# Optimization experiments

Measured on AMD Instinct MI355X. Metric: run time of the kernel, lower is better.

The kernel has to match this reference:

```python
import jax, jax.numpy as jnp
import numpy as np

B, SQ, SK = 2, 2048, 2048
D = 1024            # in_features == num_heads * head_size
H, HS = 16, 64      # num_heads, head_size
SCALE = HS ** -0.5


def setup_inputs() -> dict:
    key = jax.random.key(0)
    ks = jax.random.split(key, 10)
    s = 0.02
    return {
        "inputs": jax.random.normal(ks[0], (B, SQ, D), jnp.float32),
        "context": jax.random.normal(ks[1], (B, SK, D), jnp.float32),
        "Wq": jax.random.normal(ks[2], (D, D), jnp.float32) * s,
        "bq": jnp.zeros((D,), jnp.float32),
        "Wk": jax.random.normal(ks[3], (D, D), jnp.float32) * s,
        "bk": jnp.zeros((D,), jnp.float32),
        "Wv": jax.random.normal(ks[4], (D, D), jnp.float32) * s,
        "bv": jnp.zeros((D,), jnp.float32),
        "Wo": jax.random.normal(ks[5], (D, D), jnp.float32) * s,
        "bo": jnp.zeros((D,), jnp.float32),
    }


def reference(inputs, context, Wq, bq, Wk, bk, Wv, bv, Wo, bo):
    # QKV projections (torch Linear: x @ W.T + b; here W stored as [in, out])
    q = inputs @ Wq + bq            # [B, SQ, D]
    k = context @ Wk + bk           # [B, SK, D]
    v = context @ Wv + bv           # [B, SK, D]
    q = q.reshape(B, SQ, H, HS)
    k = k.reshape(B, SK, H, HS)
    v = v.reshape(B, SK, H, HS)
    # scores: [B, H, SQ, SK] -- full score matrix materialized (as in source)
    score = jnp.einsum("bqhd,bkhd->bhqk", q, k) * SCALE
    weights = jax.nn.softmax(score, axis=-1)
    attn = jnp.einsum("bhqk,bkhd->bqhd", weights, v)  # [B, SQ, H, HS]
    out = attn.reshape(B, SQ, H * HS)
    return out @ Wo + bo
```

## Files before the change

kernel.cpp:

```cpp
#include <hip/hip_runtime.h>

#define BB 2
#define SQ 2048
#define SK 2048
#define DD 1024
#define HH 16
#define HS 64
#define SCALE 0.125f
#define LOG2E 1.4426950408889634f

typedef __bf16 bf16x8 __attribute__((ext_vector_type(8)));
typedef float f32x4 __attribute__((ext_vector_type(4)));
typedef unsigned int uint;

#if defined(__has_builtin)
#if __has_builtin(__builtin_amdgcn_exp2f)
#define FEXP2(x) __builtin_amdgcn_exp2f(x)
#endif
#endif
#ifndef FEXP2
extern "C" __device__ float __ocml_native_exp2_f32(float);
#define FEXP2(x) __ocml_native_exp2_f32(x)
#endif

__device__ __forceinline__ void gload_lds16(const __bf16* g, __bf16* l) {
    __builtin_amdgcn_global_load_lds((const __attribute__((address_space(1))) uint*)(g),
                                     (__attribute__((address_space(3))) uint*)(l), 16, 0, 0);
}

__global__ void wtrans(const float* __restrict__ W0, const float* __restrict__ W1,
                       const float* __restrict__ W2, const float* __restrict__ W3,
                       __bf16* __restrict__ Wt) {
    __shared__ __bf16 tile[32][33];
    const float* W = blockIdx.z == 0 ? W0 : blockIdx.z == 1 ? W1 : blockIdx.z == 2 ? W2 : W3;
    __bf16* out = Wt + (size_t)blockIdx.z * DD * DD;
    int tx = threadIdx.x, ty = threadIdx.y;
    int k0 = blockIdx.y * 32, n0 = blockIdx.x * 32;
#pragma unroll
    for (int j = 0; j < 4; ++j)
        tile[ty + j * 8][tx] = (__bf16)W[(size_t)(k0 + ty + j * 8) * DD + n0 + tx];
    __syncthreads();
#pragma unroll
    for (int j = 0; j < 4; ++j) {
        int n = n0 + ty + j * 8;
        int k = k0 + tx;
        int kswz = (k & ~63) | ((((k >> 3) ^ n) & 7) << 3) | (k & 7);
        out[(size_t)n * DD + kswz] = tile[tx][ty + j * 8];
    }
}

__global__ __launch_bounds__(256, 3) void gemm_qkv(
        const float* __restrict__ Ain, const float* __restrict__ Actx,
        const __bf16* __restrict__ Wt,
        const float* __restrict__ bq, const float* __restrict__ bk, const float* __restrict__ bv,
        __bf16* __restrict__ Qb, __bf16* __restrict__ Kb, __bf16* __restrict__ Vtb,
        float qscale) {
    __shared__ __bf16 As[128 * 64];
    __shared__ __bf16 Bs[128 * 64];
    int t = threadIdx.x, w = t >> 6, l = t & 63;
    int lm = l & 15, lk = l >> 4;
    int wr = w >> 1, wc = w & 1;
    int flat = blockIdx.x + 16 * blockIdx.y;
    int nf = (flat & 7) * 96 + (flat >> 3);
    bool isQ = nf < 256;
    int bc, br;
    if (isQ) { bc = nf & 7; br = nf >> 3; }
    else     { int f = nf - 256; bc = f & 15; br = f >> 4; }

    int rA = t >> 3, cA = t & 7;
    const float* Afp = isQ ? Ain : Actx;
    const float* agb = Afp + (size_t)(br * 128 + rA) * 1024 + cA * 8;
    __bf16* aw = &As[rA * 64 + ((cA ^ (rA & 7)) * 8)];

    const __bf16 *bg0, *bg1, *bg2, *bg3;
    if (isQ) {
        const __bf16* Wq_ = Wt;
        bg0 = Wq_ + (size_t)(bc * 128 + rA)      * 1024 + cA * 8;
        bg1 = Wq_ + (size_t)(bc * 128 + rA + 32) * 1024 + cA * 8;
        bg2 = Wq_ + (size_t)(bc * 128 + rA + 64) * 1024 + cA * 8;
        bg3 = Wq_ + (size_t)(bc * 128 + rA + 96) * 1024 + cA * 8;
    } else {
        const __bf16* Wk_ = Wt + (size_t)DD * DD;
        const __bf16* Wv_ = Wt + (size_t)2 * DD * DD;
        bg0 = Wk_ + (size_t)(bc * 64 + rA)      * 1024 + cA * 8;
        bg1 = Wk_ + (size_t)(bc * 64 + rA + 32) * 1024 + cA * 8;
        bg2 = Wv_ + (size_t)(bc * 64 + rA)      * 1024 + cA * 8;
        bg3 = Wv_ + (size_t)(bc * 64 + rA + 32) * 1024 + cA * 8;
    }
    __bf16* bw = &Bs[rA * 64 + cA * 8];

    int brow[4];
#pragma unroll
    for (int n = 0; n < 4; ++n)
        brow[n] = isQ ? (wc * 64 + n * 16 + lm)
                      : ((n >> 1) * 64 + wc * 32 + (n & 1) * 16 + lm);

    float4 a0l, a0h, a1l, a1h, a2l, a2h, a3l, a3h, xb0, xb1, xb2, xb3;
#define G_LOAD()                                                                      \
    a0l = *(const float4*)(agb);              a0h = *(const float4*)(agb + 4);        \
    a1l = *(const float4*)(agb + 32768);      a1h = *(const float4*)(agb + 32772);    \
    a2l = *(const float4*)(agb + 65536);      a2h = *(const float4*)(agb + 65540);    \
    a3l = *(const float4*)(agb + 98304);      a3h = *(const float4*)(agb + 98308);    \
    xb0 = *(const float4*)bg0; xb1 = *(const float4*)bg1;                             \
    xb2 = *(const float4*)bg2; xb3 = *(const float4*)bg3;                             \
    agb += 64; bg0 += 64; bg1 += 64; bg2 += 64; bg3 += 64;
#define CVT8(LO, HI) bf16x8{(__bf16)LO.x, (__bf16)LO.y, (__bf16)LO.z, (__bf16)LO.w,   \
                            (__bf16)HI.x, (__bf16)HI.y, (__bf16)HI.z, (__bf16)HI.w}
#define G_WRITE()                                                                     \
    {                                                                                 \
        *(bf16x8*)(aw)        = CVT8(a0l, a0h);                                       \
        *(bf16x8*)(aw + 2048) = CVT8(a1l, a1h);                                       \
        *(bf16x8*)(aw + 4096) = CVT8(a2l, a2h);                                       \
        *(bf16x8*)(aw + 6144) = CVT8(a3l, a3h);                                       \
        *(float4*)(bw)        = xb0;                                                  \
        *(float4*)(bw + 2048) = xb1;                                                  \
        *(float4*)(bw + 4096) = xb2;                                                  \
        *(float4*)(bw + 6144) = xb3;                                                  \
    }

    f32x4 acc[4][4] = {};
    G_LOAD();
    for (int ts = 0; ts < 16; ++ts) {
        __syncthreads();
        G_WRITE();
        __syncthreads();
        if (ts + 1 < 16) { G_LOAD(); }
#pragma unroll
        for (int kk = 0; kk < 2; ++kk) {
            int ch = kk * 4 + lk;
            bf16x8 af[4], bf[4];
#pragma unroll
            for (int m = 0; m < 4; ++m)
                af[m] = *(const bf16x8*)&As[(wr * 64 + m * 16 + lm) * 64 + ((ch ^ (lm & 7)) * 8)];
#pragma unroll
            for (int n = 0; n < 4; ++n)
                bf[n] = *(const bf16x8*)&Bs[brow[n] * 64 + ((ch ^ (lm & 7)) * 8)];
#pragma unroll
            for (int m = 0; m < 4; ++m)
#pragma unroll
                for (int n = 0; n < 4; ++n)
                    acc[m][n] = __builtin_amdgcn_mfma_f32_16x16x32_bf16(af[m], bf[n], acc[m][n], 0, 0, 0);
        }
    }
#undef G_LOAD
#undef G_WRITE
#undef CVT8

    if (isQ) {
#pragma unroll
        for (int m = 0; m < 4; ++m)
#pragma unroll
            for (int n = 0; n < 4; ++n) {
                int col = bc * 128 + wc * 64 + n * 16 + lm;
                float bb = bq[col];
#pragma unroll
                for (int r = 0; r < 4; ++r) {
                    int row = br * 128 + wr * 64 + m * 16 + lk * 4 + r;
                    Qb[(size_t)row * 1024 + col] = (__bf16)((acc[m][n][r] + bb) * qscale);
                }
            }
    } else {
#pragma unroll
        for (int m = 0; m < 4; ++m)
#pragma unroll
            for (int n = 0; n < 4; ++n) {
                int col = bc * 64 + wc * 32 + (n & 1) * 16 + lm;
                if (n < 2) {
                    float bb = bk[col];
#pragma unroll
                    for (int r = 0; r < 4; ++r) {
                        int row = br * 128 + wr * 64 + m * 16 + lk * 4 + r;
                        Kb[(size_t)row * 1024 + col] = (__bf16)(acc[m][n][r] + bb);
                    }
                } else {
                    float bb = bv[col];
                    int row = br * 128 + wr * 64 + m * 16 + lk * 4;
                    int b_ = row >> 11, sk = row & 2047;
                    int skb = sk & ~63, o = sk & 63;
                    int p0 = (o & 32) | (((o >> 3) & 1) << 4) | (((o >> 2) & 1) << 3) | (((o >> 4) & 1) << 2);
                    int h_ = col >> 6, d_ = col & 63;
                    union { ushort4 u; __bf16 hh[4]; } pk;
#pragma unroll
                    for (int r = 0; r < 4; ++r) pk.hh[r] = (__bf16)(acc[m][n][r] + bb);
                    *(ushort4*)(Vtb + ((size_t)((b_ * 16 + h_) * 64 + d_) * 2048 + skb + p0)) = pk.u;
                }
            }
    }
}

__global__ __launch_bounds__(256) void gemm_out64(const __bf16* __restrict__ A, const __bf16* __restrict__ Bt,
                                                  const float* __restrict__ bias, float* __restrict__ C) {
    __shared__ __bf16 As[64][64];
    __shared__ __bf16 Bs[128][64];
    int t = threadIdx.x;
    int w = t >> 6, l = t & 63;
    int lm = l & 15, lk = l >> 4;
    int flat = blockIdx.x + 8 * blockIdx.y;
    int nf = (flat & 7) * 64 + (flat >> 3);
    int bc = nf & 7, br = nf >> 3;
    int srow = (l >> 3), scol = (l & 7) * 8;
    f32x4 acc[4][2] = {};
    for (int kt = 0; kt < 1024; kt += 64) {
        __syncthreads();
#pragma unroll
        for (int j = 0; j < 2; ++j) {
            int r0 = (j * 4 + w) * 8;
            gload_lds16(&A[(size_t)(br * 64 + r0 + srow) * 1024 + kt + scol], &As[r0][0]);
        }
#pragma unroll
        for (int j = 0; j < 4; ++j) {
            int r0 = (j * 4 + w) * 8;
            gload_lds16(&Bt[(size_t)(bc * 128 + r0 + srow) * 1024 + kt + scol], &Bs[r0][0]);
        }
        __syncthreads();
#pragma unroll
        for (int kk = 0; kk < 64; kk += 32) {
            int ch = ((kk >> 3) + lk);
            bf16x8 af[4], bf[2];
#pragma unroll
            for (int m = 0; m < 4; ++m) af[m] = *(const bf16x8*)&As[m * 16 + lm][kk + lk * 8];
#pragma unroll
            for (int n = 0; n < 2; ++n)
                bf[n] = *(const bf16x8*)&Bs[w * 32 + n * 16 + lm][(ch ^ (lm & 7)) * 8];
#pragma unroll
            for (int m = 0; m < 4; ++m)
#pragma unroll
                for (int n = 0; n < 2; ++n)
                    acc[m][n] = __builtin_amdgcn_mfma_f32_16x16x32_bf16(af[m], bf[n], acc[m][n], 0, 0, 0);
        }
    }
#pragma unroll
    for (int m = 0; m < 4; ++m)
#pragma unroll
        for (int n = 0; n < 2; ++n) {
            int col = bc * 128 + w * 32 + n * 16 + lm;
            float bv = bias[col];
#pragma unroll
            for (int r = 0; r < 4; ++r) {
                int row = br * 64 + m * 16 + lk * 4 + r;
                C[(size_t)row * 1024 + col] = acc[m][n][r] + bv;
            }
        }
}

__global__ __launch_bounds__(512) void flash_attn(const __bf16* __restrict__ Q,
                                                  const __bf16* __restrict__ Kb,
                                                  const __bf16* __restrict__ Vt,
                                                  __bf16* __restrict__ O) {
    __shared__ __bf16 Ks[2][64 * 64];
    __shared__ __bf16 Vs[2][64 * 64];
    int t = threadIdx.x, w = t >> 6, l = t & 63;
    int lm = l & 15, lk = l >> 4;
    int flat = blockIdx.x + 16 * blockIdx.y;
    int nf = (flat & 7) * 64 + (flat >> 3);
    int bh = nf >> 4, b = bh >> 4, h = bh & 15;
    int q0 = (nf & 15) * 128;

    bf16x8 qf[2];
#pragma unroll
    for (int kk = 0; kk < 2; ++kk)
        qf[kk] = *(const bf16x8*)&Q[(size_t)(b * SQ + q0 + w * 16 + lm) * DD + h * HS + kk * 32 + lk * 8];

    int r0 = t >> 3, c8 = t & 7;
    int chs = c8 ^ (r0 & 7);
    __bf16* ksl0 = &Ks[0][r0 * 64 + chs * 8];
    __bf16* vsl0 = &Vs[0][r0 * 64 + chs * 8];

    const __bf16* kp0 = Kb + (size_t)b * SK * DD + h * HS + (size_t)r0 * DD + c8 * 8;
    const __bf16* vp0 = Vt + (size_t)bh * HS * SK + (size_t)r0 * SK + c8 * 8;

    int o0 = lm * 64 + ((lk ^ (lm & 7)) * 8);
    int o1 = lm * 64 + (((4 + lk) ^ (lm & 7)) * 8);

    float4 kr0, vr0;
#define FA_LOAD()                                                                \
    kr0 = *(const float4*)kp0; vr0 = *(const float4*)vp0;                        \
    kp0 += (size_t)64 * DD; vp0 += 64;
#define FA_WRITE(BUF)                                                            \
    *(float4*)(ksl0 + (BUF) * 4096) = kr0;                                       \
    *(float4*)(vsl0 + (BUF) * 4096) = vr0;

    FA_LOAD();
    FA_WRITE(0);
    __syncthreads();

    bf16x8 ones;
#pragma unroll
    for (int j = 0; j < 8; ++j) ones[j] = (__bf16)1.0f;

    f32x4 o[4] = {};
    f32x4 o_s = {};

    for (int it = 0; it < 32; ++it) {
        int buf = it & 1;
        if (it + 1 < 32) { FA_LOAD(); }

        const __bf16* KsB = &Ks[buf][0];
        const __bf16* VsB = &Vs[buf][0];

        f32x4 st[4] = {};
        __builtin_amdgcn_s_setprio(1);
#pragma unroll
        for (int kk = 0; kk < 2; ++kk) {
#pragma unroll
            for (int n = 0; n < 4; ++n) {
                bf16x8 kf = *(const bf16x8*)&KsB[(kk ? o1 : o0) + n * 1024];
                st[n] = __builtin_amdgcn_mfma_f32_16x16x32_bf16(kf, qf[kk], st[n], 0, 0, 0);
            }
        }
        __builtin_amdgcn_s_setprio(0);

#pragma unroll
        for (int kk = 0; kk < 2; ++kk) {
            bf16x8 pa;
#pragma unroll
            for (int j = 0; j < 8; ++j)
                pa[j] = (__bf16)FEXP2(st[2 * kk + (j >> 2)][j & 3]);
            __builtin_amdgcn_s_setprio(1);
            o_s = __builtin_amdgcn_mfma_f32_16x16x32_bf16(pa, ones, o_s, 0, 0, 0);
#pragma unroll
            for (int dn = 0; dn < 4; ++dn) {
                bf16x8 vf = *(const bf16x8*)&VsB[(kk ? o1 : o0) + dn * 1024];
                o[dn] = __builtin_amdgcn_mfma_f32_16x16x32_bf16(pa, vf, o[dn], 0, 0, 0);
            }
            __builtin_amdgcn_s_setprio(0);
        }

        if (it + 1 < 32) { FA_WRITE(buf ^ 1); }
        __syncthreads();
    }

    f32x4 inv;
#pragma unroll
    for (int r = 0; r < 4; ++r) inv[r] = 1.f / o_s[r];
#pragma unroll
    for (int dn = 0; dn < 4; ++dn)
#pragma unroll
        for (int r = 0; r < 4; ++r) {
            int row = q0 + w * 16 + lk * 4 + r;
            int col = h * HS + dn * 16 + lm;
            O[(size_t)(b * SQ + row) * DD + col] = (__bf16)(o[dn][r] * inv[r]);
        }
}

extern "C" void kernel_launch(void* const* d_in, const int* in_sizes, int n_in,
                              void* d_out, int out_size, void* d_ws, size_t ws_size,
                              hipStream_t stream) {
    const float* inputs  = (const float*)d_in[0];
    const float* context = (const float*)d_in[1];
    const float* Wq = (const float*)d_in[2];
    const float* bq = (const float*)d_in[3];
    const float* Wk = (const float*)d_in[4];
    const float* bk = (const float*)d_in[5];
    const float* Wv = (const float*)d_in[6];
    const float* bv = (const float*)d_in[7];
    const float* Wo = (const float*)d_in[8];
    const float* bo = (const float*)d_in[9];
    float* out = (float*)d_out;

    char* ws = (char*)d_ws;
    const size_t SEG = (size_t)4096 * 1024 * sizeof(__bf16);
    __bf16* attb = (__bf16*)(ws + 0 * SEG);
    __bf16* Wt   = (__bf16*)(ws + 2 * SEG);
    __bf16* Qb   = (__bf16*)(ws + 3 * SEG);
    __bf16* Kbuf = (__bf16*)(ws + 4 * SEG);
    __bf16* Vtb  = (__bf16*)(ws + 5 * SEG);

    wtrans<<<dim3(32, 32, 4), dim3(32, 8), 0, stream>>>(Wq, Wk, Wv, Wo, Wt);

    gemm_qkv<<<dim3(16, 48), 256, 0, stream>>>(inputs, context, Wt, bq, bk, bv,
                                               Qb, Kbuf, Vtb, SCALE * LOG2E);

    flash_attn<<<dim3(16, 32), 512, 0, stream>>>(Qb, Kbuf, Vtb, attb);

    gemm_out64<<<dim3(8, 64), 256, 0, stream>>>(attb, Wt + (size_t)3 * DD * DD, bo, out);
}
```

Measured before the change: 105.2 us.

## Pre-cast activations to bf16 and stage QKV GEMM tiles via direct global-to-LDS loads

Adds a separate kernel that casts the fp32 inputs and context to bf16 in workspace. The QKV GEMM then loads A and B tiles straight into LDS with global_load_lds instead of going through registers with an in-kernel conversion. The goal is to halve the A-operand bytes re-read across column tiles and to cut register pressure and VALU conversion work. In exchange it adds a full read/write pass over both activations and drops the register prefetch overlap, so global loads are now issued between the barriers with no double buffering.

```diff
diff --git a/kernel.cpp b/kernel.cpp
--- a/kernel.cpp
+++ b/kernel.cpp
@@ -28,6 +28,21 @@
                                      (__attribute__((address_space(3))) uint*)(l), 16, 0, 0);
 }
 
+__global__ void cast2_f32_bf16(const float* __restrict__ in0, const float* __restrict__ in1,
+                               __bf16* __restrict__ out0, __bf16* __restrict__ out1, int n8each) {
+    int i = blockIdx.x * blockDim.x + threadIdx.x;
+    const float* src;
+    __bf16* dst;
+    int j;
+    if (i < n8each) { src = in0; dst = out0; j = i; }
+    else            { src = in1; dst = out1; j = i - n8each; }
+    const float4* p = ((const float4*)src) + (size_t)j * 2;
+    float4 a = p[0], b = p[1];
+    bf16x8 v = {(__bf16)a.x, (__bf16)a.y, (__bf16)a.z, (__bf16)a.w,
+                (__bf16)b.x, (__bf16)b.y, (__bf16)b.z, (__bf16)b.w};
+    ((bf16x8*)dst)[j] = v;
+}
+
 __global__ void wtrans(const float* __restrict__ W0, const float* __restrict__ W1,
                        const float* __restrict__ W2, const float* __restrict__ W3,
                        __bf16* __restrict__ Wt) {
@@ -49,8 +64,8 @@
     }
 }
 
-__global__ __launch_bounds__(256, 3) void gemm_qkv(
-        const float* __restrict__ Ain, const float* __restrict__ Actx,
+__global__ __launch_bounds__(256) void gemm_qkv(
+        const __bf16* __restrict__ Ain, const __bf16* __restrict__ Actx,
         const __bf16* __restrict__ Wt,
         const float* __restrict__ bq, const float* __restrict__ bk, const float* __restrict__ bv,
         __bf16* __restrict__ Qb, __bf16* __restrict__ Kb, __bf16* __restrict__ Vtb,
@@ -68,10 +83,8 @@
     else     { int f = nf - 256; bc = f & 15; br = f >> 4; }
 
     int rA = t >> 3, cA = t & 7;
-    const float* Afp = isQ ? Ain : Actx;
-    const float* agb = Afp + (size_t)(br * 128 + rA) * 1024 + cA * 8;
-    __bf16* aw = &As[rA * 64 + ((cA ^ (rA & 7)) * 8)];
-
+    const __bf16* ag = (isQ ? Ain : Actx) + (size_t)(br * 128 + rA) * 1024 + ((cA ^ (rA & 7)) * 8);
+    __bf16* adst = &As[rA * 64 + cA * 8];
     const __bf16 *bg0, *bg1, *bg2, *bg3;
     if (isQ) {
         const __bf16* Wq_ = Wt;
@@ -87,7 +100,7 @@
         bg2 = Wv_ + (size_t)(bc * 64 + rA)      * 1024 + cA * 8;
         bg3 = Wv_ + (size_t)(bc * 64 + rA + 32) * 1024 + cA * 8;
     }
-    __bf16* bw = &Bs[rA * 64 + cA * 8];
+    __bf16* bdst = &Bs[rA * 64 + cA * 8];
 
     int brow[4];
 #pragma unroll
@@ -95,36 +108,21 @@
         brow[n] = isQ ? (wc * 64 + n * 16 + lm)
                       : ((n >> 1) * 64 + wc * 32 + (n & 1) * 16 + lm);
 
-    float4 a0l, a0h, a1l, a1h, a2l, a2h, a3l, a3h, xb0, xb1, xb2, xb3;
-#define G_LOAD()                                                                      \
-    a0l = *(const float4*)(agb);              a0h = *(const float4*)(agb + 4);        \
-    a1l = *(const float4*)(agb + 32768);      a1h = *(const float4*)(agb + 32772);    \
-    a2l = *(const float4*)(agb + 65536);      a2h = *(const float4*)(agb + 65540);    \
-    a3l = *(const float4*)(agb + 98304);      a3h = *(const float4*)(agb + 98308);    \
-    xb0 = *(const float4*)bg0; xb1 = *(const float4*)bg1;                             \
-    xb2 = *(const float4*)bg2; xb3 = *(const float4*)bg3;                             \
-    agb += 64; bg0 += 64; bg1 += 64; bg2 += 64; bg3 += 64;
-#define CVT8(LO, HI) bf16x8{(__bf16)LO.x, (__bf16)LO.y, (__bf16)LO.z, (__bf16)LO.w,   \
-                            (__bf16)HI.x, (__bf16)HI.y, (__bf16)HI.z, (__bf16)HI.w}
-#define G_WRITE()                                                                     \
-    {                                                                                 \
-        *(bf16x8*)(aw)        = CVT8(a0l, a0h);                                       \
-        *(bf16x8*)(aw + 2048) = CVT8(a1l, a1h);                                       \
-        *(bf16x8*)(aw + 4096) = CVT8(a2l, a2h);                                       \
-        *(bf16x8*)(aw + 6144) = CVT8(a3l, a3h);                                       \
-        *(float4*)(bw)        = xb0;                                                  \
-        *(float4*)(bw + 2048) = xb1;                                                  \
-        *(float4*)(bw + 4096) = xb2;                                                  \
-        *(float4*)(bw + 6144) = xb3;                                                  \
-    }
+#define STAGE(KT)                                                                     \
+    gload_lds16(ag + (KT),               adst);                                       \
+    gload_lds16(ag + 32768 + (KT),       adst + 2048);                                \
+    gload_lds16(ag + 65536 + (KT),       adst + 4096);                                \
+    gload_lds16(ag + 98304 + (KT),       adst + 6144);                                \
+    gload_lds16(bg0 + (KT), bdst);                                                    \
+    gload_lds16(bg1 + (KT), bdst + 2048);                                             \
+    gload_lds16(bg2 + (KT), bdst + 4096);                                             \
+    gload_lds16(bg3 + (KT), bdst + 6144);
 
     f32x4 acc[4][4] = {};
-    G_LOAD();
     for (int ts = 0; ts < 16; ++ts) {
         __syncthreads();
-        G_WRITE();
-        __syncthreads();
-        if (ts + 1 < 16) { G_LOAD(); }
+        STAGE(ts * 64);
+        __syncthreads();
 #pragma unroll
         for (int kk = 0; kk < 2; ++kk) {
             int ch = kk * 4 + lk;
@@ -142,9 +140,7 @@
                     acc[m][n] = __builtin_amdgcn_mfma_f32_16x16x32_bf16(af[m], bf[n], acc[m][n], 0, 0, 0);
         }
     }
-#undef G_LOAD
-#undef G_WRITE
-#undef CVT8
+#undef STAGE
 
     if (isQ) {
 #pragma unroll
@@ -361,14 +357,18 @@
     char* ws = (char*)d_ws;
     const size_t SEG = (size_t)4096 * 1024 * sizeof(__bf16);
     __bf16* attb = (__bf16*)(ws + 0 * SEG);
+    __bf16* inA  = (__bf16*)(ws + 1 * SEG);
     __bf16* Wt   = (__bf16*)(ws + 2 * SEG);
     __bf16* Qb   = (__bf16*)(ws + 3 * SEG);
     __bf16* Kbuf = (__bf16*)(ws + 4 * SEG);
     __bf16* Vtb  = (__bf16*)(ws + 5 * SEG);
-
+    __bf16* ctxB = (__bf16*)(ws + 6 * SEG);
+
+    int n8 = 4096 * 1024 / 8;
+    cast2_f32_bf16<<<2 * n8 / 256, 256, 0, stream>>>(inputs, context, inA, ctxB, n8);
     wtrans<<<dim3(32, 32, 4), dim3(32, 8), 0, stream>>>(Wq, Wk, Wv, Wo, Wt);
 
-    gemm_qkv<<<dim3(16, 48), 256, 0, stream>>>(inputs, context, Wt, bq, bk, bv,
+    gemm_qkv<<<dim3(16, 48), 256, 0, stream>>>(inA, ctxB, Wt, bq, bk, bv,
                                                Qb, Kbuf, Vtb, SCALE * LOG2E);
 
     flash_attn<<<dim3(16, 32), 512, 0, stream>>>(Qb, Kbuf, Vtb, attb);
```

Measured after the change: 118.0 us. +12.2%, slower.

## Double-buffer QKV GEMM LDS tiles and use 512-thread blocks

Applied to the files above, without the earlier changes.

The QKV projection GEMM moves from 256 to 512 threads per block, with 8 waves arranged 2x4 so each wave holds a 64x32 accumulator tile instead of 64x64. LDS A/B tiles are double-buffered, so the next k-slice is written into the alternate buffer after the MFMAs and only one barrier per iteration is needed instead of two. The aim is to hide global-load and LDS-write latency behind compute and raise wave count. In exchange LDS per block doubles, the occupancy hint of 3 blocks is dropped, and each wave reuses fragments less.

```diff
diff --git a/kernel.cpp b/kernel.cpp
--- a/kernel.cpp
+++ b/kernel.cpp
@@ -49,17 +49,17 @@
     }
 }
 
-__global__ __launch_bounds__(256, 3) void gemm_qkv(
+__global__ __launch_bounds__(512) void gemm_qkv(
         const float* __restrict__ Ain, const float* __restrict__ Actx,
         const __bf16* __restrict__ Wt,
         const float* __restrict__ bq, const float* __restrict__ bk, const float* __restrict__ bv,
         __bf16* __restrict__ Qb, __bf16* __restrict__ Kb, __bf16* __restrict__ Vtb,
         float qscale) {
-    __shared__ __bf16 As[128 * 64];
-    __shared__ __bf16 Bs[128 * 64];
+    __shared__ __bf16 As[2 * 128 * 64];
+    __shared__ __bf16 Bs[2 * 128 * 64];
     int t = threadIdx.x, w = t >> 6, l = t & 63;
     int lm = l & 15, lk = l >> 4;
-    int wr = w >> 1, wc = w & 1;
+    int wr = w >> 2, wc = w & 3;
     int flat = blockIdx.x + 16 * blockIdx.y;
     int nf = (flat & 7) * 96 + (flat >> 3);
     bool isQ = nf < 256;
@@ -67,80 +67,61 @@
     if (isQ) { bc = nf & 7; br = nf >> 3; }
     else     { int f = nf - 256; bc = f & 15; br = f >> 4; }
 
-    int rA = t >> 3, cA = t & 7;
+    int rS = t >> 3, cS = t & 7;
     const float* Afp = isQ ? Ain : Actx;
-    const float* agb = Afp + (size_t)(br * 128 + rA) * 1024 + cA * 8;
-    __bf16* aw = &As[rA * 64 + ((cA ^ (rA & 7)) * 8)];
-
-    const __bf16 *bg0, *bg1, *bg2, *bg3;
+    const float* ag = Afp + (size_t)(br * 128 + rS) * 1024 + cS * 8;
+    __bf16* aw = &As[rS * 64 + ((cS ^ (rS & 7)) * 8)];
+    const __bf16 *bg0, *bg1;
     if (isQ) {
-        const __bf16* Wq_ = Wt;
-        bg0 = Wq_ + (size_t)(bc * 128 + rA)      * 1024 + cA * 8;
-        bg1 = Wq_ + (size_t)(bc * 128 + rA + 32) * 1024 + cA * 8;
-        bg2 = Wq_ + (size_t)(bc * 128 + rA + 64) * 1024 + cA * 8;
-        bg3 = Wq_ + (size_t)(bc * 128 + rA + 96) * 1024 + cA * 8;
+        bg0 = Wt + (size_t)(bc * 128 + rS)      * 1024 + cS * 8;
+        bg1 = Wt + (size_t)(bc * 128 + rS + 64) * 1024 + cS * 8;
     } else {
-        const __bf16* Wk_ = Wt + (size_t)DD * DD;
-        const __bf16* Wv_ = Wt + (size_t)2 * DD * DD;
-        bg0 = Wk_ + (size_t)(bc * 64 + rA)      * 1024 + cA * 8;
-        bg1 = Wk_ + (size_t)(bc * 64 + rA + 32) * 1024 + cA * 8;
-        bg2 = Wv_ + (size_t)(bc * 64 + rA)      * 1024 + cA * 8;
-        bg3 = Wv_ + (size_t)(bc * 64 + rA + 32) * 1024 + cA * 8;
-    }
-    __bf16* bw = &Bs[rA * 64 + cA * 8];
-
-    int brow[4];
-#pragma unroll
-    for (int n = 0; n < 4; ++n)
-        brow[n] = isQ ? (wc * 64 + n * 16 + lm)
-                      : ((n >> 1) * 64 + wc * 32 + (n & 1) * 16 + lm);
-
-    float4 a0l, a0h, a1l, a1h, a2l, a2h, a3l, a3h, xb0, xb1, xb2, xb3;
+        bg0 = Wt + (size_t)DD * DD     + (size_t)(bc * 64 + rS) * 1024 + cS * 8;
+        bg1 = Wt + (size_t)2 * DD * DD + (size_t)(bc * 64 + rS) * 1024 + cS * 8;
+    }
+    __bf16* bw = &Bs[rS * 64 + cS * 8];
+
+    float4 a0l, a0h, a1l, a1h, xb0, xb1;
 #define G_LOAD()                                                                      \
-    a0l = *(const float4*)(agb);              a0h = *(const float4*)(agb + 4);        \
-    a1l = *(const float4*)(agb + 32768);      a1h = *(const float4*)(agb + 32772);    \
-    a2l = *(const float4*)(agb + 65536);      a2h = *(const float4*)(agb + 65540);    \
-    a3l = *(const float4*)(agb + 98304);      a3h = *(const float4*)(agb + 98308);    \
-    xb0 = *(const float4*)bg0; xb1 = *(const float4*)bg1;                             \
-    xb2 = *(const float4*)bg2; xb3 = *(const float4*)bg3;                             \
-    agb += 64; bg0 += 64; bg1 += 64; bg2 += 64; bg3 += 64;
+    a0l = *(const float4*)(ag);           a0h = *(const float4*)(ag + 4);             \
+    a1l = *(const float4*)(ag + 65536);   a1h = *(const float4*)(ag + 65540);         \
+    xb0 = *(const float4*)bg0;            xb1 = *(const float4*)bg1;                  \
+    ag += 64; bg0 += 64; bg1 += 64;
 #define CVT8(LO, HI) bf16x8{(__bf16)LO.x, (__bf16)LO.y, (__bf16)LO.z, (__bf16)LO.w,   \
                             (__bf16)HI.x, (__bf16)HI.y, (__bf16)HI.z, (__bf16)HI.w}
-#define G_WRITE()                                                                     \
+#define G_WRITE(BUF)                                                                  \
     {                                                                                 \
-        *(bf16x8*)(aw)        = CVT8(a0l, a0h);                                       \
-        *(bf16x8*)(aw + 2048) = CVT8(a1l, a1h);                                       \
-        *(bf16x8*)(aw + 4096) = CVT8(a2l, a2h);                                       \
-        *(bf16x8*)(aw + 6144) = CVT8(a3l, a3h);                                       \
-        *(float4*)(bw)        = xb0;                                                  \
-        *(float4*)(bw + 2048) = xb1;                                                  \
-        *(float4*)(bw + 4096) = xb2;                                                  \
-        *(float4*)(bw + 6144) = xb3;                                                  \
-    }
-
-    f32x4 acc[4][4] = {};
+        *(bf16x8*)(aw + (BUF) * 8192)        = CVT8(a0l, a0h);                        \
+        *(bf16x8*)(aw + (BUF) * 8192 + 4096) = CVT8(a1l, a1h);                        \
+        *(float4*)(bw + (BUF) * 8192)        = xb0;                                   \
+        *(float4*)(bw + (BUF) * 8192 + 4096) = xb1;                                   \
+    }
+
+    f32x4 acc[4][2] = {};
     G_LOAD();
+    G_WRITE(0);
+    __syncthreads();
     for (int ts = 0; ts < 16; ++ts) {
-        __syncthreads();
-        G_WRITE();
-        __syncthreads();
+        int buf = ts & 1;
         if (ts + 1 < 16) { G_LOAD(); }
 #pragma unroll
         for (int kk = 0; kk < 2; ++kk) {
             int ch = kk * 4 + lk;
-            bf16x8 af[4], bf[4];
+            bf16x8 af[4], bf[2];
 #pragma unroll
             for (int m = 0; m < 4; ++m)
-                af[m] = *(const bf16x8*)&As[(wr * 64 + m * 16 + lm) * 64 + ((ch ^ (lm & 7)) * 8)];
-#pragma unroll
-            for (int n = 0; n < 4; ++n)
-                bf[n] = *(const bf16x8*)&Bs[brow[n] * 64 + ((ch ^ (lm & 7)) * 8)];
+                af[m] = *(const bf16x8*)&As[buf * 8192 + (wr * 64 + m * 16 + lm) * 64 + ((ch ^ (lm & 7)) * 8)];
+#pragma unroll
+            for (int n = 0; n < 2; ++n)
+                bf[n] = *(const bf16x8*)&Bs[buf * 8192 + (wc * 32 + n * 16 + lm) * 64 + ((ch ^ (lm & 7)) * 8)];
 #pragma unroll
             for (int m = 0; m < 4; ++m)
 #pragma unroll
-                for (int n = 0; n < 4; ++n)
+                for (int n = 0; n < 2; ++n)
                     acc[m][n] = __builtin_amdgcn_mfma_f32_16x16x32_bf16(af[m], bf[n], acc[m][n], 0, 0, 0);
         }
+        if (ts + 1 < 16) { G_WRITE(buf ^ 1); }
+        __syncthreads();
     }
 #undef G_LOAD
 #undef G_WRITE
@@ -150,8 +131,8 @@
 #pragma unroll
         for (int m = 0; m < 4; ++m)
 #pragma unroll
-            for (int n = 0; n < 4; ++n) {
-                int col = bc * 128 + wc * 64 + n * 16 + lm;
+            for (int n = 0; n < 2; ++n) {
+                int col = bc * 128 + wc * 32 + n * 16 + lm;
                 float bb = bq[col];
 #pragma unroll
                 for (int r = 0; r < 4; ++r) {
@@ -159,31 +140,35 @@
                     Qb[(size_t)row * 1024 + col] = (__bf16)((acc[m][n][r] + bb) * qscale);
                 }
             }
+    } else if (wc < 2) {
+#pragma unroll
+        for (int m = 0; m < 4; ++m)
+#pragma unroll
+            for (int n = 0; n < 2; ++n) {
+                int col = bc * 64 + wc * 32 + n * 16 + lm;
+                float bb = bk[col];
+#pragma unroll
+                for (int r = 0; r < 4; ++r) {
+                    int row = br * 128 + wr * 64 + m * 16 + lk * 4 + r;
+                    Kb[(size_t)row * 1024 + col] = (__bf16)(acc[m][n][r] + bb);
+                }
+            }
     } else {
 #pragma unroll
         for (int m = 0; m < 4; ++m)
 #pragma unroll
-            for (int n = 0; n < 4; ++n) {
-                int col = bc * 64 + wc * 32 + (n & 1) * 16 + lm;
-                if (n < 2) {
-                    float bb = bk[col];
-#pragma unroll
-                    for (int r = 0; r < 4; ++r) {
-                        int row = br * 128 + wr * 64 + m * 16 + lk * 4 + r;
-                        Kb[(size_t)row * 1024 + col] = (__bf16)(acc[m][n][r] + bb);
-                    }
-                } else {
-                    float bb = bv[col];
-                    int row = br * 128 + wr * 64 + m * 16 + lk * 4;
-                    int b_ = row >> 11, sk = row & 2047;
-                    int skb = sk & ~63, o = sk & 63;
-                    int p0 = (o & 32) | (((o >> 3) & 1) << 4) | (((o >> 2) & 1) << 3) | (((o >> 4) & 1) << 2);
-                    int h_ = col >> 6, d_ = col & 63;
-                    union { ushort4 u; __bf16 hh[4]; } pk;
-#pragma unroll
-                    for (int r = 0; r < 4; ++r) pk.hh[r] = (__bf16)(acc[m][n][r] + bb);
-                    *(ushort4*)(Vtb + ((size_t)((b_ * 16 + h_) * 64 + d_) * 2048 + skb + p0)) = pk.u;
-                }
+            for (int n = 0; n < 2; ++n) {
+                int col = bc * 64 + (wc - 2) * 32 + n * 16 + lm;
+                float bb = bv[col];
+                int row = br * 128 + wr * 64 + m * 16 + lk * 4;
+                int b_ = row >> 11, sk = row & 2047;
+                int skb = sk & ~63, o = sk & 63;
+                int p0 = (o & 32) | (((o >> 3) & 1) << 4) | (((o >> 2) & 1) << 3) | (((o >> 4) & 1) << 2);
+                int h_ = col >> 6, d_ = col & 63;
+                union { ushort4 u; __bf16 hh[4]; } pk;
+#pragma unroll
+                for (int r = 0; r < 4; ++r) pk.hh[r] = (__bf16)(acc[m][n][r] + bb);
+                *(ushort4*)(Vtb + ((size_t)((b_ * 16 + h_) * 64 + d_) * 2048 + skb + p0)) = pk.u;
             }
     }
 }
@@ -368,7 +353,7 @@
 
     wtrans<<<dim3(32, 32, 4), dim3(32, 8), 0, stream>>>(Wq, Wk, Wv, Wo, Wt);
 
-    gemm_qkv<<<dim3(16, 48), 256, 0, stream>>>(inputs, context, Wt, bq, bk, bv,
+    gemm_qkv<<<dim3(16, 48), 512, 0, stream>>>(inputs, context, Wt, bq, bk, bv,
                                                Qb, Kbuf, Vtb, SCALE * LOG2E);
 
     flash_attn<<<dim3(16, 32), 512, 0, stream>>>(Qb, Kbuf, Vtb, attb);
```

After: 117.9 us. 12.1% more time.
